# Kernel optimization log

Measured on AMD Instinct MI355X. Metric: run time of the kernel, lower is better.

## Reference

```python
import jax, jax.numpy as jnp
import numpy as np

# dMoE config (matches init_kwargs): D=1024, GLU ffn F=2816 (int(2*4096/3) rounded up to 256),
# E=8 experts, top_k=2, erf-GELU activation, normalize_expert_weights=0 (skip), bias added to output.
D = 1024
F = 2816
E = 8
TOP_K = 2


def setup_inputs() -> dict:
    key = jax.random.key(0)
    ks = jax.random.split(key, 6)
    std = 0.02
    x = jax.random.normal(ks[0], (2, 2048, D), dtype=jnp.float32)
    router_w = jax.random.normal(ks[1], (D, E), dtype=jnp.float32) * std
    w1 = jax.random.normal(ks[2], (E, D, F), dtype=jnp.float32) * std
    v1 = jax.random.normal(ks[3], (E, D, F), dtype=jnp.float32) * std
    w2 = jax.random.normal(ks[4], (E, F, D), dtype=jnp.float32) * std
    bias = jnp.zeros((D,), dtype=jnp.float32)
    return {"x": x, "router_w": router_w, "w1": w1, "v1": v1, "w2": w2, "bias": bias}


def reference(x, router_w, w1, v1, w2, bias):
    B, S, d = x.shape
    xt = x.reshape(B * S, d)                       # [T, D] tokens
    # Router: linear -> softmax over experts -> top-k (no weight renormalization, p=0).
    scores = jax.nn.softmax(xt @ router_w, axis=-1)          # [T, E]
    expert_weights, expert_idx = jax.lax.top_k(scores, TOP_K)  # [T, k]
    # Dropless MoE == dense per-expert GLU MLP combined with top-k weights
    # (non-selected experts get weight 0, mathematically identical to dispatch/combine).
    h = jax.nn.gelu(jnp.einsum('td,edf->tef', xt, w1), approximate=False) \
        * jnp.einsum('td,edf->tef', xt, v1)                   # [T, E, F]
    y = jnp.einsum('tef,efd->ted', h, w2)                     # [T, E, D]
    yk = jnp.take_along_axis(y, expert_idx[:, :, None], axis=1)  # [T, k, D]
    out = jnp.sum(expert_weights[:, :, None] * yk, axis=1) + bias
    return out.reshape(B, S, d)
```

## Files before the change

kernel.cpp:

```cpp
#include <hip/hip_runtime.h>
#include <hip/hip_bf16.h>
#include <math.h>

#define D_DIM 1024
#define F_DIM 2816
#define E_NUM 8

#define BM 128
#define BK 64

typedef __attribute__((ext_vector_type(4))) float f32x4;
typedef __attribute__((ext_vector_type(8))) short short8;

__device__ __forceinline__ unsigned short f2bf(float f) {
    unsigned u = __float_as_uint(f);
    u = (u + 0x7FFFu + ((u >> 16) & 1u)) >> 16;
    return (unsigned short)u;
}

__device__ __forceinline__ float gelu_erf(float z) {
    return 0.5f * z * (1.0f + erff(z * 0.70710678118654752f));
}

__device__ __forceinline__ int swz(int row, int kb) {
    return row * 128 + (kb ^ ((row & 7) << 4));
}

__device__ __forceinline__ uint4 pack8(const unsigned short* h) {
    uint4 r;
    r.x = (unsigned)h[0] | ((unsigned)h[1] << 16);
    r.y = (unsigned)h[2] | ((unsigned)h[3] << 16);
    r.z = (unsigned)h[4] | ((unsigned)h[5] << 16);
    r.w = (unsigned)h[6] | ((unsigned)h[7] << 16);
    return r;
}

__device__ __forceinline__ void gload16(const void* g, void* l) {
    __builtin_amdgcn_global_load_lds(
        (const __attribute__((address_space(1))) unsigned int*)g,
        (__attribute__((address_space(3))) unsigned int*)l,
        16, 0, 0);
}

__global__ __launch_bounds__(256) void transpose_cvt2_kernel(
    const float* __restrict__ srcA, unsigned short* __restrict__ dstA,
    const float* __restrict__ srcB, unsigned short* __restrict__ dstB,
    int R, int C)
{
    __shared__ float tile[64][65];
    int z = blockIdx.z;
    const float* s = (z < E_NUM ? srcA : srcB);
    unsigned short* d = (z < E_NUM ? dstA : dstB);
    int e = z & 7;
    s += (size_t)e * R * C;
    d += (size_t)e * R * C;
    int c0 = blockIdx.x * 64;
    int r0 = blockIdx.y * 64;
    int tid = threadIdx.x;
#pragma unroll
    for (int i = 0; i < 4; ++i) {
        int idx = tid + 256 * i;
        int r = idx >> 4, cc = (idx & 15) * 4;
        float4 v = *(const float4*)(s + (size_t)(r0 + r) * C + c0 + cc);
        tile[r][cc] = v.x; tile[r][cc + 1] = v.y; tile[r][cc + 2] = v.z; tile[r][cc + 3] = v.w;
    }
    __syncthreads();
#pragma unroll
    for (int i = 0; i < 2; ++i) {
        int idx = tid + 256 * i;
        int c = idx >> 3, rr = (idx & 7) * 8;
        unsigned short h[8];
#pragma unroll
        for (int j = 0; j < 8; ++j) h[j] = f2bf(tile[rr + j][c]);
        *(uint4*)(d + (size_t)(c0 + c) * R + r0 + rr) = pack8(h);
    }
}

__global__ __launch_bounds__(256) void transpose_cvt_kernel(
    const float* __restrict__ src, unsigned short* __restrict__ dst, int R, int C)
{
    __shared__ float tile[64][65];
    int e = blockIdx.z;
    const float* s = src + (size_t)e * R * C;
    unsigned short* d = dst + (size_t)e * R * C;
    int c0 = blockIdx.x * 64;
    int r0 = blockIdx.y * 64;
    int tid = threadIdx.x;
#pragma unroll
    for (int i = 0; i < 4; ++i) {
        int idx = tid + 256 * i;
        int r = idx >> 4, cc = (idx & 15) * 4;
        float4 v = *(const float4*)(s + (size_t)(r0 + r) * C + c0 + cc);
        tile[r][cc] = v.x; tile[r][cc + 1] = v.y; tile[r][cc + 2] = v.z; tile[r][cc + 3] = v.w;
    }
    __syncthreads();
#pragma unroll
    for (int i = 0; i < 2; ++i) {
        int idx = tid + 256 * i;
        int c = idx >> 3, rr = (idx & 7) * 8;
        unsigned short h[8];
#pragma unroll
        for (int j = 0; j < 8; ++j) h[j] = f2bf(tile[rr + j][c]);
        *(uint4*)(d + (size_t)(c0 + c) * R + r0 + rr) = pack8(h);
    }
}

__global__ __launch_bounds__(256) void router_kernel(
    const float* __restrict__ x, const float* __restrict__ rw,
    unsigned short* __restrict__ xbf, int* __restrict__ tk_idx,
    float* __restrict__ tk_w, int* __restrict__ counts)
{
    int t = blockIdx.x * 4 + (threadIdx.x >> 6);
    int lane = threadIdx.x & 63;
    const float* xr = x + (size_t)t * D_DIM;
    float acc[E_NUM];
#pragma unroll
    for (int e = 0; e < E_NUM; ++e) acc[e] = 0.f;
#pragma unroll
    for (int i = 0; i < D_DIM / 64; ++i) {
        int d = lane + 64 * i;
        float xv = xr[d];
        xbf[(size_t)t * D_DIM + d] = f2bf(xv);
        const float* rp = rw + (size_t)d * E_NUM;
#pragma unroll
        for (int e = 0; e < E_NUM; ++e) acc[e] += xv * rp[e];
    }
#pragma unroll
    for (int e = 0; e < E_NUM; ++e) {
#pragma unroll
        for (int s = 32; s > 0; s >>= 1) acc[e] += __shfl_xor(acc[e], s, 64);
    }
    float mx = acc[0];
#pragma unroll
    for (int e = 1; e < E_NUM; ++e) mx = fmaxf(mx, acc[e]);
    float p[E_NUM], se = 0.f;
#pragma unroll
    for (int e = 0; e < E_NUM; ++e) { p[e] = expf(acc[e] - mx); se += p[e]; }
    float inv = 1.f / se;
    int e1 = 0;
#pragma unroll
    for (int e = 1; e < E_NUM; ++e) if (p[e] > p[e1]) e1 = e;
    int e2 = (e1 == 0) ? 1 : 0;
#pragma unroll
    for (int e = 0; e < E_NUM; ++e) if (e != e1 && p[e] > p[e2]) e2 = e;
    if (lane == 0) {
        tk_idx[2 * t] = e1; tk_idx[2 * t + 1] = e2;
        tk_w[2 * t] = p[e1] * inv; tk_w[2 * t + 1] = p[e2] * inv;
        atomicAdd(&counts[e1], 1);
        atomicAdd(&counts[e2], 1);
    }
}

__global__ void scan_kernel(const int* __restrict__ counts, int* __restrict__ offsets,
                            int* __restrict__ cursor,
                            int* __restrict__ tile_e, int* __restrict__ tile_row,
                            int* __restrict__ n_mt)
{
    if (threadIdx.x != 0) return;
    int off = 0, nt = 0;
    for (int e = 0; e < E_NUM; ++e) {
        offsets[e] = off;
        cursor[e] = off;
        int ne = counts[e];
        int nti = (ne + BM - 1) / BM;
        for (int i = 0; i < nti; ++i) { tile_e[nt] = e; tile_row[nt] = off + i * BM; ++nt; }
        off += ne;
    }
    offsets[E_NUM] = off;
    *n_mt = nt;
}

__global__ __launch_bounds__(256) void assign_kernel(
    const int* __restrict__ tk_idx, int* __restrict__ cursor,
    int* __restrict__ pair_token, int* __restrict__ pair_pos, int T)
{
    int t = blockIdx.x * 256 + threadIdx.x;
    if (t >= T) return;
#pragma unroll
    for (int s = 0; s < 2; ++s) {
        int e = tk_idx[2 * t + s];
        int pos = atomicAdd(&cursor[e], 1);
        pair_token[pos] = t;
        pair_pos[2 * t + s] = pos;
    }
}

__global__ __launch_bounds__(512) void gemm1_glu_kernel(
    const unsigned short* __restrict__ xbf,
    const unsigned short* __restrict__ w1t, const unsigned short* __restrict__ v1t,
    const int* __restrict__ pair_token, const int* __restrict__ offsets,
    const int* __restrict__ tile_e, const int* __restrict__ tile_row,
    const int* __restrict__ n_mt,
    unsigned short* __restrict__ hbf)
{
    __shared__ __align__(16) unsigned short As[BM * BK];
    __shared__ __align__(16) unsigned short Bs[256 * BK];

    int flat = blockIdx.x + gridDim.x * blockIdx.y;
    int nwg = gridDim.x * gridDim.y;
    int L = (flat & 7) * (nwg >> 3) + (flat >> 3);
    int mt = L % gridDim.x;
    int strip = L / gridDim.x;
    if (mt >= *n_mt) return;
    int e = tile_e[mt];
    int row0 = tile_row[mt];
    int end = offsets[e + 1];
    int n0 = strip * 128;

    int tid = threadIdx.x;
    int lane = tid & 63;
    int wid = tid >> 6;
    int wr = wid >> 2, wc = wid & 3;
    int sub = lane >> 3;
    int srcoff = (((lane & 7) ^ sub) << 4);

    const unsigned short* W0 = w1t + (size_t)e * D_DIM * F_DIM;
    const unsigned short* W1 = v1t + (size_t)e * D_DIM * F_DIM;

    const char* aptr[2];
#pragma unroll
    for (int i = 0; i < 2; ++i) {
        int r = (wid * 2 + i) * 8 + sub;
        int p = row0 + r;
        if (p >= end) p = end - 1;
        aptr[i] = (const char*)(xbf + (size_t)pair_token[p] * D_DIM) + srcoff;
    }
    const char* bptr[4];
#pragma unroll
    for (int i = 0; i < 4; ++i) {
        int r = (wid * 4 + i) * 8 + sub;
        int s = (r >> 5) & 1;
        int col = n0 + (r >> 6) * 32 + (r & 31);
        const unsigned short* base = s ? W1 : W0;
        bptr[i] = (const char*)(base + (size_t)col * D_DIM) + srcoff;
    }

    f32x4 acc[4][4];
#pragma unroll
    for (int m = 0; m < 4; ++m)
#pragma unroll
        for (int n = 0; n < 4; ++n) acc[m][n] = (f32x4){0.f, 0.f, 0.f, 0.f};

    auto STAGE = [&]() {
#pragma unroll
        for (int i = 0; i < 2; ++i) {
            gload16(aptr[i], (char*)As + (wid * 2 + i) * 1024);
            aptr[i] += 128;
        }
#pragma unroll
        for (int i = 0; i < 4; ++i) {
            gload16(bptr[i], (char*)Bs + (wid * 4 + i) * 1024);
            bptr[i] += 128;
        }
    };

    const int NT = D_DIM / BK;
    for (int kt = 0; kt < NT; ++kt) {
        STAGE();
        __syncthreads();
#pragma unroll
        for (int kk = 0; kk < 2; ++kk) {
            int kb = kk * 64 + (lane >> 4) * 16;
            short8 af[4], bf[4];
#pragma unroll
            for (int m = 0; m < 4; ++m) {
                int row = wr * 64 + m * 16 + (lane & 15);
                af[m] = *(const short8*)((char*)As + swz(row, kb));
            }
#pragma unroll
            for (int n = 0; n < 4; ++n) {
                int rn = wc * 64 + n * 16 + (lane & 15);
                bf[n] = *(const short8*)((char*)Bs + swz(rn, kb));
            }
#pragma unroll
            for (int m = 0; m < 4; ++m)
#pragma unroll
                for (int n = 0; n < 4; ++n)
                    acc[m][n] = __builtin_amdgcn_mfma_f32_16x16x32_bf16(af[m], bf[n], acc[m][n], 0, 0, 0);
        }
        __syncthreads();
    }
#pragma unroll
    for (int m = 0; m < 4; ++m) {
#pragma unroll
        for (int j = 0; j < 4; ++j) {
            int rl = wr * 64 + m * 16 + (lane >> 4) * 4 + j;
            int p = row0 + rl;
            if (p < end) {
#pragma unroll
                for (int n = 0; n < 2; ++n) {
                    float z1 = acc[m][n][j];
                    float z2 = acc[m][n + 2][j];
                    int col = n0 + wc * 32 + n * 16 + (lane & 15);
                    hbf[(size_t)p * F_DIM + col] = f2bf(gelu_erf(z1) * z2);
                }
            }
        }
    }
}

__global__ __launch_bounds__(256) void gemm2_kernel(
    const unsigned short* __restrict__ hbf,
    const unsigned short* __restrict__ w2t,
    const int* __restrict__ offsets,
    const int* __restrict__ tile_e, const int* __restrict__ tile_row,
    const int* __restrict__ n_mt,
    float* __restrict__ ypair)
{
    __shared__ __align__(16) unsigned short As[BM * BK];
    __shared__ __align__(16) unsigned short Bs[128 * BK];

    int flat = blockIdx.x + gridDim.x * blockIdx.y;
    int nwg = gridDim.x * gridDim.y;
    int L = (flat & 7) * (nwg >> 3) + (flat >> 3);
    int mt = L % gridDim.x;
    int strip = L / gridDim.x;
    if (mt >= *n_mt) return;
    int e = tile_e[mt];
    int row0 = tile_row[mt];
    int end = offsets[e + 1];
    int n0 = strip * 128;

    int tid = threadIdx.x;
    int lane = tid & 63;
    int wid = tid >> 6;
    int wr = wid >> 1, wc = wid & 1;
    int sub = lane >> 3;
    int srcoff = (((lane & 7) ^ sub) << 4);

    const unsigned short* W = w2t + (size_t)e * D_DIM * F_DIM;

    const char* aptr[4];
#pragma unroll
    for (int i = 0; i < 4; ++i) {
        int r = (wid * 4 + i) * 8 + sub;
        int p = row0 + r;
        if (p >= end) p = end - 1;
        aptr[i] = (const char*)(hbf + (size_t)p * F_DIM) + srcoff;
    }
    const char* bptr[4];
#pragma unroll
    for (int i = 0; i < 4; ++i) {
        int n = (wid * 4 + i) * 8 + sub;
        bptr[i] = (const char*)(W + (size_t)(n0 + n) * F_DIM) + srcoff;
    }

    f32x4 acc[4][4];
#pragma unroll
    for (int m = 0; m < 4; ++m)
#pragma unroll
        for (int n = 0; n < 4; ++n) acc[m][n] = (f32x4){0.f, 0.f, 0.f, 0.f};

    auto STAGE = [&]() {
#pragma unroll
        for (int i = 0; i < 4; ++i) {
            gload16(aptr[i], (char*)As + (wid * 4 + i) * 1024);
            aptr[i] += 128;
            gload16(bptr[i], (char*)Bs + (wid * 4 + i) * 1024);
            bptr[i] += 128;
        }
    };

    const int NT = F_DIM / BK;
    for (int kt = 0; kt < NT; ++kt) {
        STAGE();
        __syncthreads();
#pragma unroll
        for (int kk = 0; kk < 2; ++kk) {
            int kb = kk * 64 + (lane >> 4) * 16;
            short8 af[4], bf[4];
#pragma unroll
            for (int m = 0; m < 4; ++m) {
                int row = wr * 64 + m * 16 + (lane & 15);
                af[m] = *(const short8*)((char*)As + swz(row, kb));
            }
#pragma unroll
            for (int n = 0; n < 4; ++n) {
                int rn = wc * 64 + n * 16 + (lane & 15);
                bf[n] = *(const short8*)((char*)Bs + swz(rn, kb));
            }
#pragma unroll
            for (int m = 0; m < 4; ++m)
#pragma unroll
                for (int n = 0; n < 4; ++n)
                    acc[m][n] = __builtin_amdgcn_mfma_f32_16x16x32_bf16(af[m], bf[n], acc[m][n], 0, 0, 0);
        }
        __syncthreads();
    }
#pragma unroll
    for (int m = 0; m < 4; ++m) {
#pragma unroll
        for (int j = 0; j < 4; ++j) {
            int rl = wr * 64 + m * 16 + (lane >> 4) * 4 + j;
            int p = row0 + rl;
            if (p < end) {
#pragma unroll
                for (int n = 0; n < 4; ++n)
                    ypair[(size_t)p * D_DIM + n0 + wc * 64 + n * 16 + (lane & 15)] = acc[m][n][j];
            }
        }
    }
}

__global__ __launch_bounds__(256) void combine_kernel(
    const float* __restrict__ ypair, const int* __restrict__ pair_pos,
    const float* __restrict__ tk_w, const float* __restrict__ bias,
    float* __restrict__ out, int total4)
{
    int idx = blockIdx.x * 256 + threadIdx.x;
    if (idx >= total4) return;
    int t = idx >> 8;
    int d4 = idx & 255;
    int p0 = pair_pos[2 * t], p1 = pair_pos[2 * t + 1];
    float w0 = tk_w[2 * t], w1 = tk_w[2 * t + 1];
    float4 b = ((const float4*)bias)[d4];
    float4 y0 = ((const float4*)(ypair + (size_t)p0 * D_DIM))[d4];
    float4 y1 = ((const float4*)(ypair + (size_t)p1 * D_DIM))[d4];
    float4 r;
    r.x = b.x + w0 * y0.x + w1 * y1.x;
    r.y = b.y + w0 * y0.y + w1 * y1.y;
    r.z = b.z + w0 * y0.z + w1 * y1.z;
    r.w = b.w + w0 * y0.w + w1 * y1.w;
    ((float4*)out)[idx] = r;
}

__global__ void ws_too_small_kernel(float* out, int n) {
    int i = blockIdx.x * 256 + threadIdx.x;
    if (i < n) out[i] = 12345.0f;
}

extern "C" void kernel_launch(void* const* d_in, const int* in_sizes, int n_in,
                              void* d_out, int out_size, void* d_ws, size_t ws_size,
                              hipStream_t stream) {
    const float* x    = (const float*)d_in[0];
    const float* rw   = (const float*)d_in[1];
    const float* w1   = (const float*)d_in[2];
    const float* v1   = (const float*)d_in[3];
    const float* w2   = (const float*)d_in[4];
    const float* bias = (const float*)d_in[5];
    float* out = (float*)d_out;

    int T = in_sizes[0] / D_DIM;
    int P = 2 * T;
    int maxMT = P / BM + E_NUM;

    char* p = (char*)d_ws;
    char* ws_end = p + ws_size;
    auto alloc = [&](size_t bytes) {
        char* r = p;
        p += (bytes + 255) & ~(size_t)255;
        return r;
    };
    unsigned short* xbf   = (unsigned short*)alloc((size_t)T * D_DIM * 2);
    int*   tk_idx     = (int*)alloc((size_t)T * 2 * 4);
    float* tk_w       = (float*)alloc((size_t)T * 2 * 4);
    int*   counts     = (int*)alloc(E_NUM * 4);
    int*   offsets    = (int*)alloc((E_NUM + 1) * 4);
    int*   cursor     = (int*)alloc(E_NUM * 4);
    int*   tile_e     = (int*)alloc(maxMT * 4);
    int*   tile_row   = (int*)alloc(maxMT * 4);
    int*   n_mt       = (int*)alloc(4);
    int*   pair_token = (int*)alloc((size_t)P * 4);
    int*   pair_pos   = (int*)alloc((size_t)P * 4);
    unsigned short* hbf = (unsigned short*)alloc((size_t)P * F_DIM * 2);
    float* ypair      = (float*)alloc((size_t)P * D_DIM * 4);
    unsigned short* w1t = (unsigned short*)alloc((size_t)E_NUM * D_DIM * F_DIM * 2);
    unsigned short* v1t = (unsigned short*)alloc((size_t)E_NUM * D_DIM * F_DIM * 2);
    unsigned short* w2t = (unsigned short*)alloc((size_t)E_NUM * D_DIM * F_DIM * 2);

    if (p > ws_end) {
        ws_too_small_kernel<<<(out_size + 255) / 256, 256, 0, stream>>>(out, out_size);
        return;
    }

    hipMemsetAsync(counts, 0, E_NUM * 4, stream);
    transpose_cvt2_kernel<<<dim3(F_DIM / 64, D_DIM / 64, 2 * E_NUM), 256, 0, stream>>>(
        w1, w1t, v1, v1t, D_DIM, F_DIM);
    transpose_cvt_kernel<<<dim3(D_DIM / 64, F_DIM / 64, E_NUM), 256, 0, stream>>>(w2, w2t, F_DIM, D_DIM);
    router_kernel<<<T / 4, 256, 0, stream>>>(x, rw, xbf, tk_idx, tk_w, counts);
    scan_kernel<<<1, 64, 0, stream>>>(counts, offsets, cursor, tile_e, tile_row, n_mt);
    assign_kernel<<<(T + 255) / 256, 256, 0, stream>>>(tk_idx, cursor, pair_token, pair_pos, T);
    gemm1_glu_kernel<<<dim3(maxMT, F_DIM / 128), 512, 0, stream>>>(
        xbf, w1t, v1t, pair_token, offsets, tile_e, tile_row, n_mt, hbf);
    gemm2_kernel<<<dim3(maxMT, D_DIM / 128), 256, 0, stream>>>(
        hbf, w2t, offsets, tile_e, tile_row, n_mt, ypair);
    combine_kernel<<<(T * D_DIM / 4 + 255) / 256, 256, 0, stream>>>(
        ypair, pair_pos, tk_w, bias, out, T * D_DIM / 4);
}
```

Baseline: 450.3 us.

## Double-buffer weight tiles in both expert GEMMs and widen GEMM2 to 128x256 tiles

Both grouped GEMM kernels now double-buffer the weight (B) tile in LDS. The next B tile is prefetched before the MFMA loop, and the A tile is reloaded after a mid-iteration barrier, so global weight loads overlap with compute. GEMM2 also moves to 512 threads with a 128x256 output tile, which halves its grid along N and cuts repeated reads of the h activations. The cost is more LDS per block (which may lower occupancy), two barriers per iteration, and an A load that remains exposed.

```diff
diff --git a/kernel.cpp b/kernel.cpp
--- a/kernel.cpp
+++ b/kernel.cpp
@@ -194,7 +194,7 @@
     unsigned short* __restrict__ hbf)
 {
     __shared__ __align__(16) unsigned short As[BM * BK];
-    __shared__ __align__(16) unsigned short Bs[256 * BK];
+    __shared__ __align__(16) unsigned short Bs[2][256 * BK];
 
     int flat = blockIdx.x + gridDim.x * blockIdx.y;
     int nwg = gridDim.x * gridDim.y;
@@ -241,23 +241,31 @@
 #pragma unroll
         for (int n = 0; n < 4; ++n) acc[m][n] = (f32x4){0.f, 0.f, 0.f, 0.f};
 
-    auto STAGE = [&]() {
+    auto STAGE_A = [&]() {
 #pragma unroll
         for (int i = 0; i < 2; ++i) {
             gload16(aptr[i], (char*)As + (wid * 2 + i) * 1024);
             aptr[i] += 128;
         }
+    };
+    auto STAGE_B = [&](int buf) {
 #pragma unroll
         for (int i = 0; i < 4; ++i) {
-            gload16(bptr[i], (char*)Bs + (wid * 4 + i) * 1024);
+            gload16(bptr[i], (char*)Bs[buf] + (wid * 4 + i) * 1024);
             bptr[i] += 128;
         }
     };
 
+    STAGE_A();
+    STAGE_B(0);
+    asm volatile("s_waitcnt vmcnt(0)" ::: "memory");
+    __builtin_amdgcn_s_barrier();
+
     const int NT = D_DIM / BK;
+    int bb = 0;
     for (int kt = 0; kt < NT; ++kt) {
-        STAGE();
-        __syncthreads();
+        if (kt + 1 < NT) STAGE_B(bb ^ 1);
+        const char* Bb = (const char*)Bs[bb];
 #pragma unroll
         for (int kk = 0; kk < 2; ++kk) {
             int kb = kk * 64 + (lane >> 4) * 16;
@@ -270,7 +278,7 @@
 #pragma unroll
             for (int n = 0; n < 4; ++n) {
                 int rn = wc * 64 + n * 16 + (lane & 15);
-                bf[n] = *(const short8*)((char*)Bs + swz(rn, kb));
+                bf[n] = *(const short8*)(Bb + swz(rn, kb));
             }
 #pragma unroll
             for (int m = 0; m < 4; ++m)
@@ -278,7 +286,15 @@
                 for (int n = 0; n < 4; ++n)
                     acc[m][n] = __builtin_amdgcn_mfma_f32_16x16x32_bf16(af[m], bf[n], acc[m][n], 0, 0, 0);
         }
-        __syncthreads();
+        asm volatile("s_waitcnt lgkmcnt(0)" ::: "memory");
+        __builtin_amdgcn_sched_barrier(0);
+        __builtin_amdgcn_s_barrier();
+        __builtin_amdgcn_sched_barrier(0);
+        if (kt + 1 < NT) STAGE_A();
+        asm volatile("s_waitcnt vmcnt(0)" ::: "memory");
+        __builtin_amdgcn_sched_barrier(0);
+        __builtin_amdgcn_s_barrier();
+        bb ^= 1;
     }
 #pragma unroll
     for (int m = 0; m < 4; ++m) {
@@ -299,7 +315,7 @@
     }
 }
 
-__global__ __launch_bounds__(256) void gemm2_kernel(
+__global__ __launch_bounds__(512) void gemm2_kernel(
     const unsigned short* __restrict__ hbf,
     const unsigned short* __restrict__ w2t,
     const int* __restrict__ offsets,
@@ -308,7 +324,7 @@
     float* __restrict__ ypair)
 {
     __shared__ __align__(16) unsigned short As[BM * BK];
-    __shared__ __align__(16) unsigned short Bs[128 * BK];
+    __shared__ __align__(16) unsigned short Bs[2][256 * BK];
 
     int flat = blockIdx.x + gridDim.x * blockIdx.y;
     int nwg = gridDim.x * gridDim.y;
@@ -319,21 +335,21 @@
     int e = tile_e[mt];
     int row0 = tile_row[mt];
     int end = offsets[e + 1];
-    int n0 = strip * 128;
+    int n0 = strip * 256;
 
     int tid = threadIdx.x;
     int lane = tid & 63;
     int wid = tid >> 6;
-    int wr = wid >> 1, wc = wid & 1;
+    int wr = wid >> 2, wc = wid & 3;
     int sub = lane >> 3;
     int srcoff = (((lane & 7) ^ sub) << 4);
 
     const unsigned short* W = w2t + (size_t)e * D_DIM * F_DIM;
 
-    const char* aptr[4];
-#pragma unroll
-    for (int i = 0; i < 4; ++i) {
-        int r = (wid * 4 + i) * 8 + sub;
+    const char* aptr[2];
+#pragma unroll
+    for (int i = 0; i < 2; ++i) {
+        int r = (wid * 2 + i) * 8 + sub;
         int p = row0 + r;
         if (p >= end) p = end - 1;
         aptr[i] = (const char*)(hbf + (size_t)p * F_DIM) + srcoff;
@@ -351,20 +367,31 @@
 #pragma unroll
         for (int n = 0; n < 4; ++n) acc[m][n] = (f32x4){0.f, 0.f, 0.f, 0.f};
 
-    auto STAGE = [&]() {
+    auto STAGE_A = [&]() {
+#pragma unroll
+        for (int i = 0; i < 2; ++i) {
+            gload16(aptr[i], (char*)As + (wid * 2 + i) * 1024);
+            aptr[i] += 128;
+        }
+    };
+    auto STAGE_B = [&](int buf) {
 #pragma unroll
         for (int i = 0; i < 4; ++i) {
-            gload16(aptr[i], (char*)As + (wid * 4 + i) * 1024);
-            aptr[i] += 128;
-            gload16(bptr[i], (char*)Bs + (wid * 4 + i) * 1024);
+            gload16(bptr[i], (char*)Bs[buf] + (wid * 4 + i) * 1024);
             bptr[i] += 128;
         }
     };
 
+    STAGE_A();
+    STAGE_B(0);
+    asm volatile("s_waitcnt vmcnt(0)" ::: "memory");
+    __builtin_amdgcn_s_barrier();
+
     const int NT = F_DIM / BK;
+    int bb = 0;
     for (int kt = 0; kt < NT; ++kt) {
-        STAGE();
-        __syncthreads();
+        if (kt + 1 < NT) STAGE_B(bb ^ 1);
+        const char* Bb = (const char*)Bs[bb];
 #pragma unroll
         for (int kk = 0; kk < 2; ++kk) {
             int kb = kk * 64 + (lane >> 4) * 16;
@@ -377,7 +404,7 @@
 #pragma unroll
             for (int n = 0; n < 4; ++n) {
                 int rn = wc * 64 + n * 16 + (lane & 15);
-                bf[n] = *(const short8*)((char*)Bs + swz(rn, kb));
+                bf[n] = *(const short8*)(Bb + swz(rn, kb));
             }
 #pragma unroll
             for (int m = 0; m < 4; ++m)
@@ -385,7 +412,15 @@
                 for (int n = 0; n < 4; ++n)
                     acc[m][n] = __builtin_amdgcn_mfma_f32_16x16x32_bf16(af[m], bf[n], acc[m][n], 0, 0, 0);
         }
-        __syncthreads();
+        asm volatile("s_waitcnt lgkmcnt(0)" ::: "memory");
+        __builtin_amdgcn_sched_barrier(0);
+        __builtin_amdgcn_s_barrier();
+        __builtin_amdgcn_sched_barrier(0);
+        if (kt + 1 < NT) STAGE_A();
+        asm volatile("s_waitcnt vmcnt(0)" ::: "memory");
+        __builtin_amdgcn_sched_barrier(0);
+        __builtin_amdgcn_s_barrier();
+        bb ^= 1;
     }
 #pragma unroll
     for (int m = 0; m < 4; ++m) {
@@ -482,7 +517,7 @@
     assign_kernel<<<(T + 255) / 256, 256, 0, stream>>>(tk_idx, cursor, pair_token, pair_pos, T);
     gemm1_glu_kernel<<<dim3(maxMT, F_DIM / 128), 512, 0, stream>>>(
         xbf, w1t, v1t, pair_token, offsets, tile_e, tile_row, n_mt, hbf);
-    gemm2_kernel<<<dim3(maxMT, D_DIM / 128), 256, 0, stream>>>(
+    gemm2_kernel<<<dim3(maxMT, D_DIM / 256), 512, 0, stream>>>(
         hbf, w2t, offsets, tile_e, tile_row, n_mt, ypair);
     combine_kernel<<<(T * D_DIM / 4 + 255) / 256, 256, 0, stream>>>(
         ypair, pair_pos, tk_w, bias, out, T * D_DIM / 4);
```

Measured after the change: 509.2 us. 13.1% more time.

## Widen gemm2 tiles to 128x256 with 8 waves; batch routing atomics per block

Applied to the files above, without the earlier changes.

The down-projection GEMM now uses 512 threads and a 256-column N tile per workgroup, so each A (h) tile loaded from global memory is reused across twice as many output columns and the grid has half as many strips. The assign kernel first counts expert slots in shared memory and then does one global atomicAdd per expert per block, instead of two global atomics per token. The wider tile raises LDS use and the per-workgroup working set, and it halves the number of workgroups, which may reduce occupancy or load balance. The tail of the kernel (fragment loads and epilogue) is not shown and has to match the new 4-column wave layout.

```diff
diff --git a/kernel.cpp b/kernel.cpp
--- a/kernel.cpp
+++ b/kernel.cpp
@@ -174,14 +174,30 @@
     const int* __restrict__ tk_idx, int* __restrict__ cursor,
     int* __restrict__ pair_token, int* __restrict__ pair_pos, int T)
 {
-    int t = blockIdx.x * 256 + threadIdx.x;
-    if (t >= T) return;
-#pragma unroll
-    for (int s = 0; s < 2; ++s) {
-        int e = tk_idx[2 * t + s];
-        int pos = atomicAdd(&cursor[e], 1);
-        pair_token[pos] = t;
-        pair_pos[2 * t + s] = pos;
+    __shared__ int lcnt[E_NUM];
+    __shared__ int base[E_NUM];
+    int tid = threadIdx.x;
+    if (tid < E_NUM) lcnt[tid] = 0;
+    __syncthreads();
+    int t = blockIdx.x * 256 + tid;
+    int e0 = 0, e1 = 0, o0 = 0, o1 = 0;
+    bool valid = (t < T);
+    if (valid) {
+        e0 = tk_idx[2 * t];
+        e1 = tk_idx[2 * t + 1];
+        o0 = atomicAdd(&lcnt[e0], 1);
+        o1 = atomicAdd(&lcnt[e1], 1);
+    }
+    __syncthreads();
+    if (tid < E_NUM) base[tid] = atomicAdd(&cursor[tid], lcnt[tid]);
+    __syncthreads();
+    if (valid) {
+        int p0 = base[e0] + o0;
+        int p1 = base[e1] + o1;
+        pair_token[p0] = t;
+        pair_pos[2 * t] = p0;
+        pair_token[p1] = t;
+        pair_pos[2 * t + 1] = p1;
     }
 }
 
@@ -299,7 +315,7 @@
     }
 }
 
-__global__ __launch_bounds__(256) void gemm2_kernel(
+__global__ __launch_bounds__(512) void gemm2_kernel(
     const unsigned short* __restrict__ hbf,
     const unsigned short* __restrict__ w2t,
     const int* __restrict__ offsets,
@@ -308,7 +324,7 @@
     float* __restrict__ ypair)
 {
     __shared__ __align__(16) unsigned short As[BM * BK];
-    __shared__ __align__(16) unsigned short Bs[128 * BK];
+    __shared__ __align__(16) unsigned short Bs[256 * BK];
 
     int flat = blockIdx.x + gridDim.x * blockIdx.y;
     int nwg = gridDim.x * gridDim.y;
@@ -319,21 +335,21 @@
     int e = tile_e[mt];
     int row0 = tile_row[mt];
     int end = offsets[e + 1];
-    int n0 = strip * 128;
+    int n0 = strip * 256;
 
     int tid = threadIdx.x;
     int lane = tid & 63;
     int wid = tid >> 6;
-    int wr = wid >> 1, wc = wid & 1;
+    int wr = wid >> 2, wc = wid & 3;
     int sub = lane >> 3;
     int srcoff = (((lane & 7) ^ sub) << 4);
 
     const unsigned short* W = w2t + (size_t)e * D_DIM * F_DIM;
 
-    const char* aptr[4];
-#pragma unroll
-    for (int i = 0; i < 4; ++i) {
-        int r = (wid * 4 + i) * 8 + sub;
+    const char* aptr[2];
+#pragma unroll
+    for (int i = 0; i < 2; ++i) {
+        int r = (wid * 2 + i) * 8 + sub;
         int p = row0 + r;
         if (p >= end) p = end - 1;
         aptr[i] = (const char*)(hbf + (size_t)p * F_DIM) + srcoff;
@@ -353,9 +369,12 @@
 
     auto STAGE = [&]() {
 #pragma unroll
+        for (int i = 0; i < 2; ++i) {
+            gload16(aptr[i], (char*)As + (wid * 2 + i) * 1024);
+            aptr[i] += 128;
+        }
+#pragma unroll
         for (int i = 0; i < 4; ++i) {
-            gload16(aptr[i], (char*)As + (wid * 4 + i) * 1024);
-            aptr[i] += 128;
             gload16(bptr[i], (char*)Bs + (wid * 4 + i) * 1024);
             bptr[i] += 128;
         }
@@ -482,7 +501,7 @@
     assign_kernel<<<(T + 255) / 256, 256, 0, stream>>>(tk_idx, cursor, pair_token, pair_pos, T);
     gemm1_glu_kernel<<<dim3(maxMT, F_DIM / 128), 512, 0, stream>>>(
         xbf, w1t, v1t, pair_token, offsets, tile_e, tile_row, n_mt, hbf);
-    gemm2_kernel<<<dim3(maxMT, D_DIM / 128), 256, 0, stream>>>(
+    gemm2_kernel<<<dim3(maxMT, D_DIM / 256), 512, 0, stream>>>(
         hbf, w2t, offsets, tile_e, tile_row, n_mt, ypair);
     combine_kernel<<<(T * D_DIM / 4 + 255) / 256, 256, 0, stream>>>(
         ypair, pair_pos, tk_w, bias, out, T * D_DIM / 4);
```

Measured after the change: 411.0 us. 1.1x faster.
